# Optimization experiments

Hardware: AMD Instinct MI355X
Metric: run time of the kernel (lower is better)

## Reference

```python
import jax, jax.numpy as jnp
import numpy as np
from jax import lax

B, C, H, W = 32, 32, 64, 64
K = 1024
DN_T = ('NCHW', 'IOHW', 'NCHW')  # conv_transpose: kernel [in, out, kh, kw]
DN_C = ('NCHW', 'OIHW', 'NCHW')  # conv:           kernel [out, in, kh, kw]


def setup_inputs() -> dict:
    key = jax.random.key(0)
    ks = jax.random.split(key, 8)
    return {
        'z': jax.random.normal(ks[0], (B, C, H, W), jnp.float32),
        'codebook': jax.random.normal(ks[1], (K, C), jnp.float32),
        'w1': jax.random.normal(ks[2], (32, 128, 4, 4), jnp.float32) * 0.05,
        'b1': jnp.zeros((128,), jnp.float32),
        'w2': jax.random.normal(ks[3], (128, 64, 4, 4), jnp.float32) * 0.05,
        'b2': jnp.zeros((64,), jnp.float32),
        'w3': jax.random.normal(ks[4], (3, 64, 3, 3), jnp.float32) * 0.05,
        'b3': jnp.zeros((3,), jnp.float32),
    }


def _quantize(z, codebook):
    # z: [B, C, H, W] -> flat [N, C]
    zf = jnp.transpose(z, (0, 2, 3, 1)).reshape(-1, z.shape[1])
    # squared distances: ||z||^2 - 2 z.E^T + ||E||^2  -> [N, K]
    d = (jnp.sum(zf * zf, axis=1, keepdims=True)
         - 2.0 * zf @ codebook.T
         + jnp.sum(codebook * codebook, axis=1))
    idx = jnp.argmin(d, axis=1)                      # [N]
    q = codebook[idx].reshape(z.shape[0], z.shape[2], z.shape[3], z.shape[1])
    q = jnp.transpose(q, (0, 3, 1, 2))               # [B, C, H, W]
    # straight-through estimator
    return z + lax.stop_gradient(q - z)


def _decode(q, w1, b1, w2, b2, w3, b3):
    x = lax.conv_transpose(q, w1, strides=(2, 2), padding='SAME',
                           dimension_numbers=DN_T) + b1[None, :, None, None]
    x = jax.nn.relu(x)                               # [B, 128, 2H, 2W]
    x = lax.conv_transpose(x, w2, strides=(2, 2), padding='SAME',
                           dimension_numbers=DN_T) + b2[None, :, None, None]
    x = jax.nn.relu(x)                               # [B, 64, 4H, 4W]
    x = lax.conv_general_dilated(x, w3, window_strides=(1, 1), padding='SAME',
                                 dimension_numbers=DN_C) + b3[None, :, None, None]
    return jax.nn.sigmoid(x)                         # [B, 3, 4H, 4W]


def reference(z, codebook, w1, b1, w2, b2, w3, b3):
    q = _quantize(z, codebook)
    return _decode(q, w1, b1, w2, b2, w3, b3)
```

## Files before the change

### kernel.cpp

```cpp
#include <hip/hip_runtime.h>
#include <hip/hip_bf16.h>


typedef __attribute__((ext_vector_type(8)))  short  bf16x8;
typedef __attribute__((ext_vector_type(4)))  float  f32x4;
typedef __attribute__((ext_vector_type(16))) float  f32x16;

static constexpr int B_=32, C_=32, H_=64, W_=64, K_=1024;
static constexpr int NPOS = B_*H_*W_;

__device__ __forceinline__ unsigned short f2bf(float f){
  unsigned u = __float_as_uint(f);
  u = u + 0x7FFFu + ((u>>16)&1u);
  return (unsigned short)(u>>16);
}
__device__ __forceinline__ float bf2f(unsigned short h){
  return __uint_as_float(((unsigned)h)<<16);
}
__device__ __forceinline__ f32x16 mfma32(bf16x8 a, bf16x8 b, f32x16 c){
  return __builtin_amdgcn_mfma_f32_32x32x16_bf16(a,b,c,0,0,0);
}
__device__ __forceinline__ f32x4 mfma16(bf16x8 a, bf16x8 b, f32x4 c){
  return __builtin_amdgcn_mfma_f32_16x16x32_bf16(a,b,c,0,0,0);
}
__device__ __forceinline__ void gload16(const void* g, void* l){
  __builtin_amdgcn_global_load_lds(
      (const __attribute__((address_space(1))) void*)(unsigned long long)g,
      (__attribute__((address_space(3))) void*)(unsigned)(unsigned long long)l,
      16, 0, 0);
}
#define WAITVM(N) asm volatile("s_waitcnt vmcnt(" #N ")" ::: "memory")
__device__ __forceinline__ void barrier_raw(){
  asm volatile("" ::: "memory");
  __builtin_amdgcn_s_barrier();
  asm volatile("" ::: "memory");
}

__global__ __launch_bounds__(256) void prep_kernel(
    const float* __restrict__ cb, const float* __restrict__ w1,
    const float* __restrict__ w2, const float* __restrict__ w3,
    double* __restrict__ cb64, double* __restrict__ e2,
    unsigned short* __restrict__ cbp_hi, unsigned short* __restrict__ cbp_lo,
    float* __restrict__ e2h,
    unsigned short* __restrict__ wt1p, unsigned short* __restrict__ wt2p,
    unsigned short* __restrict__ w3p, float* __restrict__ zpage,
    int* __restrict__ cnt) {
  int idx = blockIdx.x*256 + threadIdx.x;
  if (idx == 0) cnt[0] = 0;
  if (idx < 64) zpage[idx] = 0.f;
  if (idx < K_*C_) {
    float v = cb[idx];
    cb64[idx] = (double)v;
    unsigned short h = f2bf(v);
    cbp_hi[idx] = h;
    cbp_lo[idx] = f2bf(v - bf2f(h));
  }
  if (idx < K_) {
    double s = 0.0;
    #pragma unroll
    for (int c=0;c<C_;++c){ double v=(double)cb[idx*C_+c]; s+=v*v; }
    e2[idx] = s;
    e2h[idx] = -0.5f * (float)s;
  }
  if (idx < 65536) {
    int e=idx&7, lane=(idx>>3)&63, g=(idx>>9)&3, t=(idx>>11)&3, c=(idx>>13)&1, p=idx>>14;
    int ic = c*16 + (lane>>5)*8 + e;
    int oc = g*32 + (lane&31);
    int ky = 2*(t>>1) + (p>>1), kx = 2*(t&1) + (p&1);
    wt1p[idx] = f2bf(w1[((ic*128+oc)*4+ky)*4+kx]);
  }
  if (idx < 131072) {
    int e=idx&7, lane=(idx>>3)&63, g=(idx>>9)&1, t=(idx>>10)&3, c=(idx>>12)&3, m=(idx>>14)&1, p=idx>>15;
    int ic = m*64 + c*16 + (lane>>5)*8 + e;
    int oc = g*32 + (lane&31);
    int ky = 2*(t>>1) + (p>>1), kx = 2*(t&1) + (p&1);
    wt2p[idx] = f2bf(w2[((ic*64+oc)*4+ky)*4+kx]);
  }
  if (idx < 9216) {
    int e=idx&7, lane=(idx>>3)&63, c=(idx>>9)&1, t=idx>>10;
    int ic = c*32 + ((lane>>4)&3)*8 + e;
    int oc = lane&15;
    int dy = t/3, dx = t - 3*dy;
    w3p[idx] = (oc<3) ? f2bf(w3[((oc*64+ic)*3+dy)*3+dx]) : (unsigned short)0;
  }
}

__global__ __launch_bounds__(256) void zprep_kernel(
    const float* __restrict__ z, unsigned short* __restrict__ zth,
    unsigned short* __restrict__ ztl) {
  int n = blockIdx.x*256 + threadIdx.x;
  int b = n >> 12, hw = n & 4095;
  const float* zp = z + (((size_t)b*C_) << 12) + hw;
  unsigned short th[C_], tl[C_];
  #pragma unroll
  for (int c=0;c<C_;++c) {
    float v = zp[(size_t)c<<12];
    unsigned short h = f2bf(v);
    th[c] = h;
    tl[c] = f2bf(v - bf2f(h));
  }
  bf16x8* dh = (bf16x8*)(zth + (size_t)n*C_);
  bf16x8* dl = (bf16x8*)(ztl + (size_t)n*C_);
  #pragma unroll
  for (int v=0;v<4;++v){ dh[v]=((bf16x8*)th)[v]; dl[v]=((bf16x8*)tl)[v]; }
}

__global__ __launch_bounds__(256) void quantm_kernel(
    const unsigned short* __restrict__ zth, const unsigned short* __restrict__ ztl,
    const unsigned short* __restrict__ cbp_hi, const unsigned short* __restrict__ cbp_lo,
    const float* __restrict__ e2h, const float* __restrict__ cb,
    unsigned short* __restrict__ q, int* __restrict__ cnt, int* __restrict__ list) {
  __shared__ bf16x8 ch[1024], cl[1024];
  __shared__ float  el[256];
  int tid = threadIdx.x, lane = tid&63, wv = tid>>6;
  int m0 = blockIdx.x*128 + wv*32;
  int colL = lane&15, g = lane>>4;

  bf16x8 ah[2], al[2];
  #pragma unroll
  for (int mt=0;mt<2;++mt) {
    int pos = m0 + mt*16 + colL;
    ah[mt] = *(const bf16x8*)(zth + (size_t)pos*C_ + g*8);
    al[mt] = *(const bf16x8*)(ztl + (size_t)pos*C_ + g*8);
  }

  float b1[2][4], b2[2][4]; int i1[2][4];
  #pragma unroll
  for (int mt=0;mt<2;++mt)
    #pragma unroll
    for (int r=0;r<4;++r){ b1[mt][r]=-3e38f; b2[mt][r]=-3e38f; i1[mt][r]=0; }

  for (int cb0 = 0; cb0 < K_; cb0 += 256) {
    __syncthreads();
    {
      const bf16x8* sh = (const bf16x8*)cbp_hi + cb0*4;
      const bf16x8* sl = (const bf16x8*)cbp_lo + cb0*4;
      #pragma unroll
      for (int v=0;v<4;++v){ ch[tid + v*256] = sh[tid + v*256];
                             cl[tid + v*256] = sl[tid + v*256]; }
      el[tid] = e2h[cb0 + tid];
    }
    __syncthreads();
    #pragma unroll
    for (int nt=0; nt<16; ++nt) {
      int cloc = nt*16 + colL;
      float ei = el[cloc];
      bf16x8 bh = ch[cloc*4 + g];
      bf16x8 bl = cl[cloc*4 + g];
      int nidx = cb0 + cloc;
      #pragma unroll
      for (int mt=0;mt<2;++mt) {
        f32x4 acc = {ei, ei, ei, ei};
        acc = mfma16(al[mt], bh, acc);
        acc = mfma16(ah[mt], bl, acc);
        acc = mfma16(ah[mt], bh, acc);
        #pragma unroll
        for (int r=0;r<4;++r) {
          float s = acc[r];
          b2[mt][r] = fmaxf(b2[mt][r], fminf(s, b1[mt][r]));
          if (s > b1[mt][r]) { b1[mt][r] = s; i1[mt][r] = nidx; }
        }
      }
    }
  }

  #pragma unroll
  for (int mask=1; mask<16; mask<<=1) {
    #pragma unroll
    for (int mt=0;mt<2;++mt)
      #pragma unroll
      for (int r=0;r<4;++r) {
        float o1 = __shfl_xor(b1[mt][r], mask);
        float o2 = __shfl_xor(b2[mt][r], mask);
        int   oi = __shfl_xor(i1[mt][r], mask);
        float nb2 = fmaxf(fminf(b1[mt][r], o1), fmaxf(b2[mt][r], o2));
        if (o1 > b1[mt][r]) { b1[mt][r] = o1; i1[mt][r] = oi; }
        b2[mt][r] = nb2;
      }
  }

  #pragma unroll
  for (int mt=0;mt<2;++mt)
    #pragma unroll
    for (int r=0;r<4;++r) {
      int m = m0 + mt*16 + g*4 + r;
      int idx = i1[mt][r];
      unsigned h0 = f2bf(cb[idx*C_ + 2*colL]);
      unsigned h1 = f2bf(cb[idx*C_ + 2*colL + 1]);
      ((unsigned*)q)[(((size_t)(colL>>2))*NPOS + m)*4 + (colL&3)] = h0 | (h1<<16);
      if (colL == 0 && (b1[mt][r] - b2[mt][r]) < 0.02f) {
        int slot = atomicAdd(cnt, 1);
        list[slot] = m;
      }
    }
}

__global__ __launch_bounds__(256) void refine_kernel(
    const int* __restrict__ cnt, const int* __restrict__ list,
    const float* __restrict__ z, const double* __restrict__ cb64,
    const double* __restrict__ e2, const float* __restrict__ cb,
    unsigned short* __restrict__ q) {
  int lane = threadIdx.x & 63;
  int wv = (blockIdx.x*256 + threadIdx.x) >> 6;
  int n_ref = cnt[0];
  for (int w = wv; w < n_ref; w += 1024) {
    int m = list[w];
    int b = m >> 12, hw = m & 4095;
    const float* zp = z + (((size_t)b*C_) << 12) + hw;
    double zr[C_];
    #pragma unroll
    for (int c=0;c<C_;++c) zr[c] = (double)zp[(size_t)c<<12];
    double best = -1e300; int bi = 0;
    for (int kk=0; kk<16; ++kk) {
      int k = kk*64 + lane;
      const double* e = cb64 + k*C_;
      double a0=0,a1=0,a2=0,a3=0;
      #pragma unroll
      for (int c=0;c<C_;c+=4) {
        a0 += zr[c  ]*e[c  ]; a1 += zr[c+1]*e[c+1];
        a2 += zr[c+2]*e[c+2]; a3 += zr[c+3]*e[c+3];
      }
      double s = 2.0*((a0+a1)+(a2+a3)) - e2[k];
      if (s > best) { best = s; bi = k; }
    }
    #pragma unroll
    for (int mask=1; mask<64; mask<<=1) {
      double ob = __shfl_xor(best, mask);
      int    oi = __shfl_xor(bi, mask);
      if (ob > best || (ob == best && oi < bi)) { best = ob; bi = oi; }
    }
    if (lane < 16) {
      unsigned h0 = f2bf(cb[bi*C_ + 2*lane]);
      unsigned h1 = f2bf(cb[bi*C_ + 2*lane + 1]);
      ((unsigned*)q)[(((size_t)(lane>>2))*NPOS + m)*4 + (lane&3)] = h0 | (h1<<16);
    }
  }
}

__global__ __launch_bounds__(256) void convt1_kernel(
    const unsigned short* __restrict__ q, const unsigned short* __restrict__ wt1p,
    const float* __restrict__ b1, const float* __restrict__ zpage,
    unsigned short* __restrict__ x1, int b0) {
  __shared__ unsigned short At[4*4*34*8];
  int tid = threadIdx.x;
  int p = tid>>6, py=(tid>>7)&1, px=(tid>>6)&1;
  int lane = tid&63, xi = lane&31, half = lane>>5, ocl = lane&31;
  int bl = blockIdx.z, b = b0 + bl;
  int Y0 = blockIdx.y*2, X0 = blockIdx.x*32;

  for (int s = tid; s < 544; s += 256) {
    int t = (s*1928)>>16;
    int c = s - t*34;
    int r = t & 3, k8 = t >> 2;
    int hg = Y0-1+r, wg = X0-1+c;
    const unsigned short* src =
        (hg>=0 && hg<64 && wg>=0 && wg<64)
            ? q + ((size_t)k8*NPOS + ((b<<12) + hg*64 + wg))*8
            : (const unsigned short*)zpage;
    *(bf16x8*)&At[s*8] = *(const bf16x8*)src;
  }
  __syncthreads();

  f32x16 acc[2][4];
  #pragma unroll
  for (int g=0;g<4;++g){
    float bv = b1[g*32+ocl];
    #pragma unroll
    for (int yr=0;yr<2;++yr){
      #pragma unroll
      for (int r=0;r<16;++r) acc[yr][g][r]=bv;
    }
  }

  #pragma unroll
  for (int c16=0;c16<2;++c16) {
    #pragma unroll
    for (int t=0;t<4;++t) {
      int j=t>>1, kx=t&1;
      int col = xi+px+kx;
      int rb = (c16*2+half)*4 + py + j;
      bf16x8 a0 = *(const bf16x8*)&At[((rb+0)*34+col)*8];
      bf16x8 a1 = *(const bf16x8*)&At[((rb+1)*34+col)*8];
      const unsigned short* wb = wt1p + ((size_t)(((p*2+c16)*4+t)*4)*64 + lane)*8;
      #pragma unroll
      for (int g=0;g<4;++g) {
        bf16x8 bf = *(const bf16x8*)(wb + g*512);
        acc[0][g] = mfma32(a0, bf, acc[0][g]);
        acc[1][g] = mfma32(a1, bf, acc[1][g]);
      }
    }
  }

  #pragma unroll
  for (int yr=0;yr<2;++yr) {
    int Y = 2*(Y0+yr)+py;
    #pragma unroll
    for (int g=0;g<4;++g) {
      int oc = g*32 + ocl, cg = oc>>3, o8 = oc&7;
      unsigned short* dst = x1 + ((((size_t)bl*16 + cg)*128 + Y)*128 + (2*X0+px))*8 + o8;
      #pragma unroll
      for (int r=0;r<16;++r) {
        int xo = (r&3) + 8*(r>>2) + 4*half;
        dst[(size_t)xo*16] = f2bf(fmaxf(acc[yr][g][r], 0.f));
      }
    }
  }
}

__global__ __launch_bounds__(512, 4) void convt2_kernel(
    const unsigned short* __restrict__ x1, const unsigned short* __restrict__ wt2p,
    const float* __restrict__ b2, const float* __restrict__ zpage,
    unsigned short* __restrict__ x2) {
  __shared__ unsigned short At[4*1024*8];
  int tid = threadIdx.x;
  int wv = __builtin_amdgcn_readfirstlane(tid>>6);
  int lane = tid&63;
  int p = wv>>1, yh = wv&1;
  int py = p>>1, px = p&1;
  int xi = lane&31, half = lane>>5, ocl = lane&31;
  int bl = blockIdx.z;
  int Y0 = blockIdx.y*4, X0 = blockIdx.x*32;

  auto issue = [&](int P) {
    int m = P>>1, h = P&1;
    const unsigned short* xsrc = x1 + ((size_t)bl*16 + m*8 + h*4)*128*128*8;
    #pragma unroll
    for (int it = 0; it < 2; ++it) {
      int u0 = it*512 + wv*64;
      int u = u0 + lane;
      int tl = (u*1928)>>16;
      int c  = u - tl*34;
      int k8 = (tl*43)>>8;
      int r  = tl - k8*6;
      int hg = Y0-1+r, wg = X0-1+c;
      bool v = (u < 816) && hg>=0 && hg<128 && wg>=0 && wg<128;
      const void* src = v ? (const void*)(xsrc + (((size_t)k8*128 + hg)*128 + wg)*8)
                          : (const void*)zpage;
      gload16(src, (void*)&At[((size_t)P*1024 + u0)*8]);
    }
  };

  f32x16 acc[2][2];
  #pragma unroll
  for (int g=0;g<2;++g){
    float bv = b2[g*32+ocl];
    #pragma unroll
    for (int yr=0;yr<2;++yr)
      #pragma unroll
      for (int r=0;r<16;++r) acc[yr][g][r]=bv;
  }

  auto compute = [&](int P) {
    int m = P>>1;
    const unsigned short* Ab = &At[(size_t)P*1024*8];
    #pragma unroll
    for (int ci=0; ci<2; ++ci) {
      int c16 = (P&1)*2 + ci;
      #pragma unroll
      for (int t=0;t<4;++t) {
        int j=t>>1, kx=t&1;
        int col = xi+px+kx;
        int lrow = ((c16*2+half)&3)*6 + py + j + yh*2;
        bf16x8 a0 = *(const bf16x8*)&Ab[((lrow+0)*34+col)*8];
        bf16x8 a1 = *(const bf16x8*)&Ab[((lrow+1)*34+col)*8];
        const unsigned short* wb = wt2p + ((size_t)(((((p*2+m)*4+c16)*4+t)*2))*64 + lane)*8;
        bf16x8 bf0 = *(const bf16x8*)wb;
        bf16x8 bf1 = *(const bf16x8*)(wb + 512);
        acc[0][0]=mfma32(a0,bf0,acc[0][0]); acc[1][0]=mfma32(a1,bf0,acc[1][0]);
        acc[0][1]=mfma32(a0,bf1,acc[0][1]); acc[1][1]=mfma32(a1,bf1,acc[1][1]);
      }
    }
  };

  issue(0); issue(1); issue(2);
  WAITVM(4); barrier_raw();
  compute(0);
  issue(3);
  WAITVM(4); barrier_raw();
  compute(1);
  WAITVM(2); barrier_raw();
  compute(2);
  WAITVM(0); barrier_raw();
  compute(3);

  #pragma unroll
  for (int yr=0;yr<2;++yr) {
    int Y = 2*(Y0 + yh*2 + yr) + py;
    #pragma unroll
    for (int g=0;g<2;++g) {
      int oc = g*32 + ocl, cg = oc>>3, o8 = oc&7;
      unsigned short* dst = x2 + ((((size_t)bl*8 + cg)*256 + Y)*256 + (2*X0+px))*8 + o8;
      #pragma unroll
      for (int r=0;r<16;++r) {
        int xo = (r&3) + 8*(r>>2) + 4*half;
        dst[(size_t)xo*16] = f2bf(fmaxf(acc[yr][g][r], 0.f));
      }
    }
  }
}

__global__ __launch_bounds__(256) void conv3_kernel(
    const unsigned short* __restrict__ x2, const unsigned short* __restrict__ w3p,
    const float* __restrict__ b3, const float* __restrict__ zpage,
    float* __restrict__ out, int b0) {
  __shared__ unsigned short Xt[4*6*66*8];
  int tid = threadIdx.x, w = tid>>6, lane = tid&63;
  int xi = lane&15, k8A = (lane>>4)&3, oc = lane&15;
  int bl = blockIdx.z, b = b0 + bl;
  int y0 = blockIdx.y*4, x0 = blockIdx.x*64;
  int y = y0 + w;

  f32x4 acc[4];
  float bv = (oc<3) ? b3[oc] : 0.f;
  #pragma unroll
  for (int mt=0;mt<4;++mt){ acc[mt][0]=bv; acc[mt][1]=bv; acc[mt][2]=bv; acc[mt][3]=bv; }

  for (int c=0;c<2;++c) {
    __syncthreads();
    for (int s = tid; s < 1584; s += 256) {
      int t = (s*993)>>16;
      int cc = s - t*66;
      int k8 = (t*43)>>8;
      int r = t - k8*6;
      int rf = y0-1+r, cf = x0-1+cc;
      const unsigned short* src =
          (rf>=0 && rf<256 && cf>=0 && cf<256)
              ? x2 + ((((size_t)bl*8 + c*4 + k8)*256 + rf)*256 + cf)*8
              : (const unsigned short*)zpage;
      *(bf16x8*)&Xt[s*8] = *(const bf16x8*)src;
    }
    __syncthreads();

    #pragma unroll
    for (int t=0;t<9;++t) {
      int dy = t/3, dx = t - 3*dy;
      bf16x8 bf = *(const bf16x8*)(w3p + ((size_t)(t*2+c)*64 + lane)*8);
      #pragma unroll
      for (int mt=0;mt<4;++mt) {
        bf16x8 a = *(const bf16x8*)&Xt[((size_t)(k8A*6 + (w+dy))*66 + (mt*16 + xi + dx))*8];
        acc[mt] = mfma16(a, bf, acc[mt]);
      }
    }
  }

  if (oc < 3) {
    #pragma unroll
    for (int mt=0;mt<4;++mt) {
      f32x4 v;
      #pragma unroll
      for (int r=0;r<4;++r) v[r] = 1.f/(1.f + __expf(-acc[mt][r]));
      int x = x0 + mt*16 + ((lane>>4)&3)*4;
      *(f32x4*)(out + (((size_t)b*3 + oc)*256 + y)*256 + x) = v;
    }
  }
}

extern "C" void kernel_launch(void* const* d_in, const int* in_sizes, int n_in,
                              void* d_out, int out_size, void* d_ws, size_t ws_size,
                              hipStream_t stream) {
  const float* z  = (const float*)d_in[0];
  const float* cb = (const float*)d_in[1];
  const float* w1 = (const float*)d_in[2];
  const float* b1 = (const float*)d_in[3];
  const float* w2 = (const float*)d_in[4];
  const float* b2 = (const float*)d_in[5];
  const float* w3 = (const float*)d_in[6];
  const float* b3 = (const float*)d_in[7];
  float* out = (float*)d_out;

  char* ws = (char*)d_ws;
  size_t off = 0;
  auto alloc = [&](size_t bytes) -> void* {
    void* p = (void*)(ws + off);
    off += (bytes + 255) & ~(size_t)255;
    return p;
  };
  double* cb64         = (double*)alloc((size_t)K_*C_*8);
  double* e2           = (double*)alloc((size_t)K_*8);
  float*  zpage        = (float*)alloc(256);
  unsigned short* cbph = (unsigned short*)alloc((size_t)K_*C_*2);
  unsigned short* cbpl = (unsigned short*)alloc((size_t)K_*C_*2);
  float*  e2h          = (float*)alloc((size_t)K_*4);
  int*    cnt          = (int*)alloc(256);
  int*    list         = (int*)alloc((size_t)NPOS*4);
  unsigned short* zth  = (unsigned short*)alloc((size_t)NPOS*C_*2);
  unsigned short* ztl  = (unsigned short*)alloc((size_t)NPOS*C_*2);
  unsigned short* wt1p = (unsigned short*)alloc((size_t)65536*2);
  unsigned short* wt2p = (unsigned short*)alloc((size_t)131072*2);
  unsigned short* w3p  = (unsigned short*)alloc((size_t)9216*2);
  unsigned short* q    = (unsigned short*)alloc((size_t)NPOS*C_*2);
  size_t fixed = off;

  size_t per_b = ((size_t)16*128*128*8 + (size_t)8*256*256*8) * 2;
  long long avail = (long long)ws_size - (long long)fixed;
  int chunk = (avail >= (long long)per_b) ? (int)(avail / (long long)per_b) : 1;
  if (chunk > B_) chunk = B_;
  unsigned short* x1 = (unsigned short*)alloc((size_t)chunk*16*128*128*8*2);
  unsigned short* x2 = (unsigned short*)alloc((size_t)chunk*8*256*256*8*2);

  prep_kernel<<<512, 256, 0, stream>>>(cb, w1, w2, w3, cb64, e2, cbph, cbpl,
                                       e2h, wt1p, wt2p, w3p, zpage, cnt);
  zprep_kernel<<<512, 256, 0, stream>>>(z, zth, ztl);
  quantm_kernel<<<1024, 256, 0, stream>>>(zth, ztl, cbph, cbpl, e2h, cb,
                                          q, cnt, list);
  refine_kernel<<<256, 256, 0, stream>>>(cnt, list, z, cb64, e2, cb, q);

  for (int b0 = 0; b0 < B_; b0 += chunk) {
    int nb = (B_ - b0 < chunk) ? (B_ - b0) : chunk;
    convt1_kernel<<<dim3(2,32,nb), 256, 0, stream>>>(q, wt1p, b1, zpage, x1, b0);
    convt2_kernel<<<dim3(4,32,nb), 512, 0, stream>>>(x1, wt2p, b2, zpage, x2);
    conv3_kernel <<<dim3(4,64,nb), 256, 0, stream>>>(x2, w3p, b3, zpage, out, b0);
  }
}
```

Before: 519.1 us.

## Deepen convt2 pipeline to eight LDS stages with register-prefetched weights

Splits the convt2 input staging into eight smaller shared-memory stages with a rolling three-deep prefetch and precomputed per-thread source addresses. Weight fragments are prefetched into double-buffered registers one stage ahead instead of being loaded inline just before each MFMA. The aim is to hide global-load latency and cut address arithmetic. In exchange it uses more registers, lowering the occupancy hint from 4 to 3 blocks, and adds more barriers.

```diff
diff --git a/kernel.cpp b/kernel.cpp
--- a/kernel.cpp
+++ b/kernel.cpp
@@ -307,11 +307,11 @@
   }
 }
 
-__global__ __launch_bounds__(512, 4) void convt2_kernel(
+__global__ __launch_bounds__(512, 3) void convt2_kernel(
     const unsigned short* __restrict__ x1, const unsigned short* __restrict__ wt2p,
     const float* __restrict__ b2, const float* __restrict__ zpage,
     unsigned short* __restrict__ x2) {
-  __shared__ unsigned short At[4*1024*8];
+  __shared__ unsigned short At[8*512*8];
   int tid = threadIdx.x;
   int wv = __builtin_amdgcn_readfirstlane(tid>>6);
   int lane = tid&63;
@@ -321,23 +321,30 @@
   int bl = blockIdx.z;
   int Y0 = blockIdx.y*4, X0 = blockIdx.x*32;
 
-  auto issue = [&](int P) {
-    int m = P>>1, h = P&1;
-    const unsigned short* xsrc = x1 + ((size_t)bl*16 + m*8 + h*4)*128*128*8;
-    #pragma unroll
-    for (int it = 0; it < 2; ++it) {
-      int u0 = it*512 + wv*64;
-      int u = u0 + lane;
-      int tl = (u*1928)>>16;
-      int c  = u - tl*34;
-      int k8 = (tl*43)>>8;
-      int r  = tl - k8*6;
-      int hg = Y0-1+r, wg = X0-1+c;
-      bool v = (u < 816) && hg>=0 && hg<128 && wg>=0 && wg<128;
-      const void* src = v ? (const void*)(xsrc + (((size_t)k8*128 + hg)*128 + wg)*8)
+  int u = wv*64 + lane;
+  int k8l = (u*322)>>16;
+  int rem = u - 204*k8l;
+  int row = (rem*1928)>>16;
+  int col = rem - 34*row;
+  int hg = Y0-1+row, wg = X0-1+col;
+  bool inb = (u < 408) && hg>=0 && hg<128 && wg>=0 && wg<128;
+  const unsigned short* sbase = inb
+      ? x1 + (((size_t)(bl*16 + k8l)*128 + hg)*128 + wg)*8
+      : (const unsigned short*)zpage;
+
+  auto SLOAD = [&](int sp) {
+    const void* src = inb ? (const void*)(sbase + (size_t)((sp>>2)*8 + (sp&3)*2)*131072)
                           : (const void*)zpage;
-      gload16(src, (void*)&At[((size_t)P*1024 + u0)*8]);
-    }
+    gload16(src, (void*)&At[(sp*512 + wv*64)*8]);
+  };
+
+  const unsigned short* wbase = wt2p + ((size_t)p*2*4*4*2)*512 + lane*8;
+  auto WLOAD = [&](int sp, bf16x8* buf) {
+    int m = sp>>2, c16 = sp&3;
+    const unsigned short* wb = wbase + (size_t)((m*4 + c16)*4)*2*512;
+    #pragma unroll
+    for (int i=0;i<8;++i)
+      buf[i] = *(const bf16x8*)(wb + (size_t)i*512);
   };
 
   f32x16 acc[2][2];
@@ -350,38 +357,39 @@
       for (int r=0;r<16;++r) acc[yr][g][r]=bv;
   }
 
-  auto compute = [&](int P) {
-    int m = P>>1;
-    const unsigned short* Ab = &At[(size_t)P*1024*8];
-    #pragma unroll
-    for (int ci=0; ci<2; ++ci) {
-      int c16 = (P&1)*2 + ci;
-      #pragma unroll
-      for (int t=0;t<4;++t) {
-        int j=t>>1, kx=t&1;
-        int col = xi+px+kx;
-        int lrow = ((c16*2+half)&3)*6 + py + j + yh*2;
-        bf16x8 a0 = *(const bf16x8*)&Ab[((lrow+0)*34+col)*8];
-        bf16x8 a1 = *(const bf16x8*)&Ab[((lrow+1)*34+col)*8];
-        const unsigned short* wb = wt2p + ((size_t)(((((p*2+m)*4+c16)*4+t)*2))*64 + lane)*8;
-        bf16x8 bf0 = *(const bf16x8*)wb;
-        bf16x8 bf1 = *(const bf16x8*)(wb + 512);
-        acc[0][0]=mfma32(a0,bf0,acc[0][0]); acc[1][0]=mfma32(a1,bf0,acc[1][0]);
-        acc[0][1]=mfma32(a0,bf1,acc[0][1]); acc[1][1]=mfma32(a1,bf1,acc[1][1]);
-      }
+  auto COMPUTE = [&](int sp, const bf16x8* buf) {
+    const unsigned short* Ab = &At[(size_t)sp*512*8];
+    #pragma unroll
+    for (int t=0;t<4;++t) {
+      int j=t>>1, kx=t&1;
+      int cA = xi+px+kx;
+      int r0 = half*204 + (py + j + yh*2)*34 + cA;
+      bf16x8 a0 = *(const bf16x8*)&Ab[(r0     )*8];
+      bf16x8 a1 = *(const bf16x8*)&Ab[(r0 + 34)*8];
+      acc[0][0]=mfma32(a0,buf[t*2  ],acc[0][0]); acc[1][0]=mfma32(a1,buf[t*2  ],acc[1][0]);
+      acc[0][1]=mfma32(a0,buf[t*2+1],acc[0][1]); acc[1][1]=mfma32(a1,buf[t*2+1],acc[1][1]);
     }
   };
 
-  issue(0); issue(1); issue(2);
-  WAITVM(4); barrier_raw();
-  compute(0);
-  issue(3);
-  WAITVM(4); barrier_raw();
-  compute(1);
-  WAITVM(2); barrier_raw();
-  compute(2);
-  WAITVM(0); barrier_raw();
-  compute(3);
+  bf16x8 wA[8], wB[8];
+  SLOAD(0); WLOAD(0, wA); SLOAD(1); WLOAD(1, wB); SLOAD(2);
+
+  WAITVM(10); barrier_raw();
+  COMPUTE(0, wA); SLOAD(3); WLOAD(2, wA);
+  WAITVM(10); barrier_raw();
+  COMPUTE(1, wB); SLOAD(4); WLOAD(3, wB);
+  WAITVM(9);  barrier_raw();
+  COMPUTE(2, wA); SLOAD(5); WLOAD(4, wA);
+  WAITVM(9);  barrier_raw();
+  COMPUTE(3, wB); SLOAD(6); WLOAD(5, wB);
+  WAITVM(9);  barrier_raw();
+  COMPUTE(4, wA); SLOAD(7); WLOAD(6, wA);
+  WAITVM(9);  barrier_raw();
+  COMPUTE(5, wB); WLOAD(7, wB);
+  WAITVM(8);  barrier_raw();
+  COMPUTE(6, wA);
+  WAITVM(0);  barrier_raw();
+  COMPUTE(7, wB);
 
   #pragma unroll
   for (int yr=0;yr<2;++yr) {
```

New measurement: 520.0 us. No clear change (+0.2%).

## Enlarge conv3 tile to 8 rows, add XCD swizzle and MFMA priority hints

Applied to the files above, without the earlier changes.

Each conv3 block now computes 8 output rows instead of 4, with two rows per wave. This loads a 10-row halo per tile instead of 6, so there is less redundant halo traffic, and it halves the grid. Block IDs are remapped so that neighbouring tiles land on the same XCD, for L2 locality. In convt2, s_setprio raises wave priority around the MFMA compute section. The cost is more accumulator registers and fewer blocks in flight.

```diff
diff --git a/kernel.cpp b/kernel.cpp
--- a/kernel.cpp
+++ b/kernel.cpp
@@ -34,6 +34,11 @@
   asm volatile("" ::: "memory");
   __builtin_amdgcn_s_barrier();
   asm volatile("" ::: "memory");
+}
+__device__ __forceinline__ int xcd_swz(int lid, int nwg){
+  int q = nwg >> 3, r = nwg & 7;
+  int xcd = lid & 7, pos = lid >> 3;
+  return (xcd < r ? xcd*(q+1) : r*(q+1) + (xcd-r)*q) + pos;
 }
 
 __global__ __launch_bounds__(256) void prep_kernel(
@@ -353,6 +358,7 @@
   auto compute = [&](int P) {
     int m = P>>1;
     const unsigned short* Ab = &At[(size_t)P*1024*8];
+    __builtin_amdgcn_s_setprio(1);
     #pragma unroll
     for (int ci=0; ci<2; ++ci) {
       int c16 = (P&1)*2 + ci;
@@ -370,6 +376,7 @@
         acc[0][1]=mfma32(a0,bf1,acc[0][1]); acc[1][1]=mfma32(a1,bf1,acc[1][1]);
       }
     }
+    __builtin_amdgcn_s_setprio(0);
   };
 
   issue(0); issue(1); issue(2);
@@ -403,25 +410,34 @@
     const unsigned short* __restrict__ x2, const unsigned short* __restrict__ w3p,
     const float* __restrict__ b3, const float* __restrict__ zpage,
     float* __restrict__ out, int b0) {
-  __shared__ unsigned short Xt[4*6*66*8];
+  __shared__ unsigned short Xt[2640*8];
   int tid = threadIdx.x, w = tid>>6, lane = tid&63;
   int xi = lane&15, k8A = (lane>>4)&3, oc = lane&15;
-  int bl = blockIdx.z, b = b0 + bl;
-  int y0 = blockIdx.y*4, x0 = blockIdx.x*64;
-  int y = y0 + w;
-
-  f32x4 acc[4];
+
+  int gx = gridDim.x, gy = gridDim.y;
+  int nwg = gx*gy*(int)gridDim.z;
+  int lid = blockIdx.x + gx*(blockIdx.y + gy*blockIdx.z);
+  int swz = xcd_swz(lid, nwg);
+  int bx = swz % gx; int t2 = swz / gx; int by = t2 % gy; int bl = t2 / gy;
+
+  int b = b0 + bl;
+  int y0 = by*8, x0 = bx*64;
+
+  f32x4 acc[2][4];
   float bv = (oc<3) ? b3[oc] : 0.f;
   #pragma unroll
-  for (int mt=0;mt<4;++mt){ acc[mt][0]=bv; acc[mt][1]=bv; acc[mt][2]=bv; acc[mt][3]=bv; }
+  for (int dr=0;dr<2;++dr)
+    #pragma unroll
+    for (int mt=0;mt<4;++mt){ acc[dr][mt][0]=bv; acc[dr][mt][1]=bv;
+                              acc[dr][mt][2]=bv; acc[dr][mt][3]=bv; }
 
   for (int c=0;c<2;++c) {
     __syncthreads();
-    for (int s = tid; s < 1584; s += 256) {
+    for (int s = tid; s < 2640; s += 256) {
       int t = (s*993)>>16;
       int cc = s - t*66;
-      int k8 = (t*43)>>8;
-      int r = t - k8*6;
+      int k8 = (t*26)>>8;
+      int r = t - k8*10;
       int rf = y0-1+r, cf = x0-1+cc;
       const unsigned short* src =
           (rf>=0 && rf<256 && cf>=0 && cf<256)
@@ -436,21 +452,29 @@
       int dy = t/3, dx = t - 3*dy;
       bf16x8 bf = *(const bf16x8*)(w3p + ((size_t)(t*2+c)*64 + lane)*8);
       #pragma unroll
+      for (int dr=0;dr<2;++dr) {
+        int row = w*2 + dr + dy;
+        #pragma unroll
+        for (int mt=0;mt<4;++mt) {
+          bf16x8 a = *(const bf16x8*)&Xt[((size_t)(k8A*10 + row)*66 + (mt*16 + xi + dx))*8];
+          acc[dr][mt] = mfma16(a, bf, acc[dr][mt]);
+        }
+      }
+    }
+  }
+
+  if (oc < 3) {
+    #pragma unroll
+    for (int dr=0;dr<2;++dr) {
+      int y = y0 + w*2 + dr;
+      #pragma unroll
       for (int mt=0;mt<4;++mt) {
-        bf16x8 a = *(const bf16x8*)&Xt[((size_t)(k8A*6 + (w+dy))*66 + (mt*16 + xi + dx))*8];
-        acc[mt] = mfma16(a, bf, acc[mt]);
-      }
-    }
-  }
-
-  if (oc < 3) {
-    #pragma unroll
-    for (int mt=0;mt<4;++mt) {
-      f32x4 v;
-      #pragma unroll
-      for (int r=0;r<4;++r) v[r] = 1.f/(1.f + __expf(-acc[mt][r]));
-      int x = x0 + mt*16 + ((lane>>4)&3)*4;
-      *(f32x4*)(out + (((size_t)b*3 + oc)*256 + y)*256 + x) = v;
+        f32x4 v;
+        #pragma unroll
+        for (int r=0;r<4;++r) v[r] = 1.f/(1.f + __expf(-acc[dr][mt][r]));
+        int x = x0 + mt*16 + ((lane>>4)&3)*4;
+        *(f32x4*)(out + (((size_t)b*3 + oc)*256 + y)*256 + x) = v;
+      }
     }
   }
 }
@@ -509,6 +533,6 @@
     int nb = (B_ - b0 < chunk) ? (B_ - b0) : chunk;
     convt1_kernel<<<dim3(2,32,nb), 256, 0, stream>>>(q, wt1p, b1, zpage, x1, b0);
     convt2_kernel<<<dim3(4,32,nb), 512, 0, stream>>>(x1, wt2p, b2, zpage, x2);
-    conv3_kernel <<<dim3(4,64,nb), 256, 0, stream>>>(x2, w3p, b3, zpage, out, b0);
-  }
-}
+    conv3_kernel <<<dim3(4,32,nb), 256, 0, stream>>>(x2, w3p, b3, zpage, out, b0);
+  }
+}
```

Measured after the change: 525.4 us. About the same (+1.2%).
